# Performance work log

Measured on AMD Instinct MI355X. Metric: run time of the kernel, lower is better.

## Reference

```python
import jax, jax.numpy as jnp
import numpy as np

B, LA, LQ, LO, H, OUT = 32, 2048, 64, 32, 1024, 5


def _kaiming(key, out_f, in_f):
    return jax.random.normal(key, (out_f, in_f), jnp.float32) * np.sqrt(2.0 / in_f)


def setup_inputs() -> dict:
    key = jax.random.key(0)
    ks = jax.random.split(key, 16)
    inp = {
        "article_contexts": jax.random.normal(ks[0], (B, LA, H), jnp.float32),
        "question_contexts": jax.random.normal(ks[1], (B, LQ, H), jnp.float32),
        "options_embeds": jax.random.normal(ks[2], (B, 5, LO, H), jnp.float32),
        "answer_indices": jax.random.randint(ks[3], (B,), 0, LQ),
    }
    # mlp_att (article-question attention) params
    inp["a_Qw"], inp["a_Qb"] = _kaiming(ks[4], H, H), jnp.zeros((H,), jnp.float32)
    inp["a_Kw"], inp["a_Kb"] = _kaiming(ks[5], H, H), jnp.zeros((H,), jnp.float32)
    inp["a_Vw"], inp["a_Vb"] = _kaiming(ks[6], H, H), jnp.zeros((H,), jnp.float32)
    inp["a_vw"], inp["a_vb"] = _kaiming(ks[7], 1, H), jnp.zeros((1,), jnp.float32)
    # dot_layer (option attention) params
    inp["d_Qw"], inp["d_Qb"] = _kaiming(ks[8], H, H), jnp.zeros((H,), jnp.float32)
    inp["d_Kw"], inp["d_Kb"] = _kaiming(ks[9], H, H), jnp.zeros((H,), jnp.float32)
    inp["d_Vw"], inp["d_Vb"] = _kaiming(ks[10], H, H), jnp.zeros((H,), jnp.float32)
    inp["d_vw"], inp["d_vb"] = _kaiming(ks[11], 1, H), jnp.zeros((1,), jnp.float32)
    # final linear: hidden_size*5 -> output_dim
    inp["f_w"], inp["f_b"] = _kaiming(ks[12], OUT, 5 * H), jnp.zeros((OUT,), jnp.float32)
    return inp


def _mlp_att(Q, K, V, Qw, Qb, Kw, Kb, Vw, Vb, vw, vb):
    # Q: [B, H]; K, V: [B, (..opt..), L, H]. Dropout is identity (eval mode).
    Qp = Q @ Qw.T + Qb                      # [B, H]
    Kp = K @ Kw.T + Kb                      # [..., L, H]
    Vp = V @ Vw.T + Vb                      # [..., L, H]
    while Qp.ndim < Kp.ndim:
        Qp = Qp[..., None, :]
    M = jnp.tanh(Qp + Kp)                   # [..., L, H]
    scores = jax.nn.softmax(M @ vw.T + vb, axis=-2)  # softmax over L, [..., L, 1]
    return jnp.sum(Vp * scores, axis=-2)    # [..., H]


def reference(article_contexts, question_contexts, options_embeds, answer_indices,
              a_Qw, a_Qb, a_Kw, a_Kb, a_Vw, a_Vb, a_vw, a_vb,
              d_Qw, d_Qb, d_Kw, d_Kb, d_Vw, d_Vb, d_vw, d_vb,
              f_w, f_b):
    b = article_contexts.shape[0]
    # gather question context at the answer index -> [B, H]
    oqc = question_contexts[jnp.arange(b), answer_indices]
    # article-question additive attention -> [B, H]
    aq = _mlp_att(oqc, article_contexts, article_contexts,
                  a_Qw, a_Qb, a_Kw, a_Kb, a_Vw, a_Vb, a_vw, a_vb)
    # per-option additive attention, vectorized over the 5 options -> [B, 5, H]
    feats = _mlp_att(aq, options_embeds, options_embeds,
                     d_Qw, d_Qb, d_Kw, d_Kb, d_Vw, d_Vb, d_vw, d_vb)
    # concat options along feature dim, final linear -> [B, OUT]
    logits = feats.reshape(b, -1) @ f_w.T + f_b
    return logits
```

## Files before the change

### kernel.cpp

```cpp
#include <hip/hip_runtime.h>
#include <hip/hip_bf16.h>
#include <math.h>

#define HDIM 1024
#define NB 32
#define LA 2048
#define LO 32

typedef __attribute__((ext_vector_type(8))) short bf16x8;
typedef __attribute__((ext_vector_type(4))) float f32x4;
typedef unsigned int u32;

__device__ __forceinline__ float tanh_fast(float x){
    return 2.0f / (1.0f + __expf(-2.0f * x)) - 1.0f;
}

__device__ __forceinline__ void load_lds16(const void* gptr, void* lptr){
    __builtin_amdgcn_global_load_lds(
        (const __attribute__((address_space(1))) u32*)gptr,
        (__attribute__((address_space(3))) u32*)lptr, 16, 0, 0);
}

__global__ void zero_kernel(float* __restrict__ p, int n){
    int i = blockIdx.x * blockDim.x + threadIdx.x;
    int stride = gridDim.x * blockDim.x;
    for (; i < n; i += stride) p[i] = 0.0f;
}

__global__ void conv_bf16_kernel(const float* __restrict__ in, __hip_bfloat16* __restrict__ out, long n){
    long i = ((long)blockIdx.x * blockDim.x + threadIdx.x) * 4;
    long stride = (long)gridDim.x * blockDim.x * 4;
    for (; i < n; i += stride){
        float4 v = *(const float4*)(in + i);
        union { __hip_bfloat16 h[4]; short4 s; } u;
        u.h[0] = __float2bfloat16(v.x); u.h[1] = __float2bfloat16(v.y);
        u.h[2] = __float2bfloat16(v.z); u.h[3] = __float2bfloat16(v.w);
        *(short4*)(out + i) = u.s;
    }
}

__global__ void gather_kernel(const float* __restrict__ qc, const int* __restrict__ ans,
                              float* __restrict__ oqc){
    int b = blockIdx.x, tid = threadIdx.x;
    int idx = ans[b];
    const float* src = qc + ((size_t)b * 64 + idx) * HDIM;
    float* dst = oqc + (size_t)b * HDIM;
    #pragma unroll
    for (int l = 0; l < 4; l++) dst[tid + l * 256] = src[tid + l * 256];
}

__global__ __launch_bounds__(256) void proj_kernel(
    const float* __restrict__ in, const float* __restrict__ W,
    const float* __restrict__ bias, float* __restrict__ out){
    __shared__ float xin[HDIM];
    const int g = blockIdx.x, tid = threadIdx.x;
    const int lane = tid & 63, wave = tid >> 6;
    *(float4*)&xin[tid * 4] = *(const float4*)&in[(size_t)g * HDIM + tid * 4];
    __syncthreads();
    float4 xv[4];
    #pragma unroll
    for (int c = 0; c < 4; c++) xv[c] = *(const float4*)&xin[(c * 64 + lane) * 4];
    const int hbase = blockIdx.y * 64 + wave * 16;
    #pragma unroll 4
    for (int r = 0; r < 16; r++){
        int h = hbase + r;
        const float* Wr = W + (size_t)h * HDIM;
        float p = 0.f;
        #pragma unroll
        for (int c = 0; c < 4; c++){
            float4 wv = *(const float4*)&Wr[(c * 64 + lane) * 4];
            p = fmaf(xv[c].x, wv.x, p); p = fmaf(xv[c].y, wv.y, p);
            p = fmaf(xv[c].z, wv.z, p); p = fmaf(xv[c].w, wv.w, p);
        }
        #pragma unroll
        for (int off = 1; off < 64; off <<= 1) p += __shfl_xor(p, off, 64);
        if (lane == 0) out[(size_t)g * HDIM + h] = p + bias[h];
    }
}

#define NT 16
__global__ __launch_bounds__(512, 4) void score_mfma128_kernel(
    const __hip_bfloat16* __restrict__ X, const __hip_bfloat16* __restrict__ Kw,
    const float* __restrict__ Kb, const float* __restrict__ Qp,
    const float* __restrict__ vw, float* __restrict__ s,
    int row_off, int rows_per_batch)
{
    __shared__ __align__(16) char lds[65536];
    const int tid = threadIdx.x;
    const int lane = tid & 63, wid = tid >> 6;
    const int wm = wid >> 2, wn = wid & 3;
    const int lr = lane & 15, lg = lane >> 4;

    const int na = gridDim.x >> 3;
    const int per = na >> 3;
    const int bid = blockIdx.x;
    const int xcd = bid & 7, seq = bid >> 3;
    const int a_idx = xcd * per + (seq >> 3);
    const int h_idx = seq & 7;
    const int a0 = a_idx * 128;
    const int h0 = h_idx * 128;

    f32x4 acc[4][2] = {};

    const int rw_c0 = tid >> 3,  srcb_c0 = ((tid & 7) * 16) ^ ((rw_c0 & 7) << 4);
    const int rw_c1 = rw_c0 + 64, srcb_c1 = ((tid & 7) * 16) ^ ((rw_c1 & 7) << 4);
    const char* pA0 = (const char*)Kw + (size_t)(h0 + rw_c0) * 2048 + srcb_c0;
    const char* pA1 = (const char*)Kw + (size_t)(h0 + rw_c1) * 2048 + srcb_c1;
    const char* pB0 = (const char*)X  + (size_t)(a0 + rw_c0) * 2048 + srcb_c0;
    const char* pB1 = (const char*)X  + (size_t)(a0 + rw_c1) * 2048 + srcb_c1;
    char* dA0 = lds + tid * 16;
    char* dA1 = lds + 8192 + tid * 16;
    char* dB0 = lds + 32768 + tid * 16;
    char* dB1 = lds + 32768 + 8192 + tid * 16;

    int aoff[4][2], boff[2][2];
    #pragma unroll
    for (int hf = 0; hf < 4; hf++){
        int rw = wm * 64 + hf * 16 + lr;
        int o0 = rw * 128 + ((lg * 16) ^ ((rw & 7) << 4));
        aoff[hf][0] = o0; aoff[hf][1] = o0 ^ 64;
    }
    #pragma unroll
    for (int af = 0; af < 2; af++){
        int rw = wn * 32 + af * 16 + lr;
        int o0 = 32768 + rw * 128 + ((lg * 16) ^ ((rw & 7) << 4));
        boff[af][0] = o0; boff[af][1] = o0 ^ 64;
    }

#define STAGE_ADV(bufoff) do { \
    load_lds16(pA0, dA0 + (bufoff)); load_lds16(pA1, dA1 + (bufoff)); \
    load_lds16(pB0, dB0 + (bufoff)); load_lds16(pB1, dB1 + (bufoff)); \
    pA0 += 128; pA1 += 128; pB0 += 128; pB1 += 128; } while(0)

#define COMPUTE(bufoff) do { \
    _Pragma("unroll") \
    for (int ks = 0; ks < 2; ks++){ \
        bf16x8 av[4], bv[2]; \
        _Pragma("unroll") \
        for (int hf = 0; hf < 4; hf++) \
            av[hf] = *(const bf16x8*)(lds + (bufoff) + aoff[hf][ks]); \
        _Pragma("unroll") \
        for (int af = 0; af < 2; af++) \
            bv[af] = *(const bf16x8*)(lds + (bufoff) + boff[af][ks]); \
        __builtin_amdgcn_s_setprio(1); \
        _Pragma("unroll") \
        for (int hf = 0; hf < 4; hf++) \
            _Pragma("unroll") \
            for (int af = 0; af < 2; af++) \
                acc[hf][af] = __builtin_amdgcn_mfma_f32_16x16x32_bf16(av[hf], bv[af], acc[hf][af], 0, 0, 0); \
        __builtin_amdgcn_s_setprio(0); \
    } } while(0)

    STAGE_ADV(0);
    STAGE_ADV(16384);
    int bo = 0;
    for (int kt = 0; kt < NT - 1; ++kt){
        asm volatile("s_waitcnt vmcnt(4)" ::: "memory");
        __builtin_amdgcn_s_barrier();
        __builtin_amdgcn_sched_barrier(0);
        COMPUTE(bo);
        __builtin_amdgcn_s_barrier();
        if (kt < NT - 2) STAGE_ADV(bo);
        bo ^= 16384;
    }
    asm volatile("s_waitcnt vmcnt(0)" ::: "memory");
    __builtin_amdgcn_s_barrier();
    __builtin_amdgcn_sched_barrier(0);
    COMPUTE(bo);

    const int b = (row_off + a0) / rows_per_batch;
    float qv[4][4], vv[4][4];
    #pragma unroll
    for (int hf = 0; hf < 4; hf++){
        int hbase = h0 + wm * 64 + hf * 16 + lg * 4;
        float4 kb4 = *(const float4*)(Kb + hbase);
        float4 qp4 = *(const float4*)(Qp + (size_t)b * HDIM + hbase);
        float4 vw4 = *(const float4*)(vw + hbase);
        qv[hf][0] = kb4.x + qp4.x; qv[hf][1] = kb4.y + qp4.y;
        qv[hf][2] = kb4.z + qp4.z; qv[hf][3] = kb4.w + qp4.w;
        vv[hf][0] = vw4.x; vv[hf][1] = vw4.y; vv[hf][2] = vw4.z; vv[hf][3] = vw4.w;
    }
    #pragma unroll
    for (int af = 0; af < 2; af++){
        float sacc = 0.f;
        #pragma unroll
        for (int hf = 0; hf < 4; hf++)
            #pragma unroll
            for (int r = 0; r < 4; r++)
                sacc += tanh_fast(acc[hf][af][r] + qv[hf][r]) * vv[hf][r];
        sacc += __shfl_xor(sacc, 16, 64);
        sacc += __shfl_xor(sacc, 32, 64);
        if (lane < 16)
            atomicAdd(&s[row_off + a0 + wn * 32 + af * 16 + lr], sacc);
    }
#undef STAGE_ADV
#undef COMPUTE
}

#define SBM 128
#define SBN 128
__global__ __launch_bounds__(256) void score_mfma_kernel(
    const __hip_bfloat16* __restrict__ X, const __hip_bfloat16* __restrict__ Kw,
    const float* __restrict__ Kb, const float* __restrict__ Qp,
    const float* __restrict__ vw, float* __restrict__ s,
    int row_off, int rows_per_batch)
{
    __shared__ __align__(16) __hip_bfloat16 As[SBM][32];
    __shared__ __align__(16) __hip_bfloat16 Bs[SBN][32];
    const int tid = threadIdx.x;
    const int lane = tid & 63, wid = tid >> 6;
    const int wm = wid >> 1, wn = wid & 1;
    const int row0 = blockIdx.x * SBM;
    const int h0 = blockIdx.y * SBN;
    const int lr = lane & 15, lg = lane >> 4;

    f32x4 acc[4][4] = {};

    for (int k0 = 0; k0 < HDIM; k0 += 32){
        #pragma unroll
        for (int l = 0; l < 2; l++){
            int f = tid + l * 256;
            int r = f >> 2, c8 = (f & 3) * 8;
            load_lds16(X + (size_t)(row0 + r) * HDIM + k0 + c8, &As[0][0] + f * 8);
            load_lds16(Kw + (size_t)(h0 + r) * HDIM + k0 + c8, &Bs[0][0] + f * 8);
        }
        __syncthreads();
        bf16x8 a[4], b[4];
        #pragma unroll
        for (int i = 0; i < 4; i++)
            a[i] = *(const bf16x8*)&As[wm * 64 + i * 16 + lr][lg * 8];
        #pragma unroll
        for (int j = 0; j < 4; j++)
            b[j] = *(const bf16x8*)&Bs[wn * 64 + j * 16 + lr][lg * 8];
        #pragma unroll
        for (int i = 0; i < 4; i++)
            #pragma unroll
            for (int j = 0; j < 4; j++)
                acc[i][j] = __builtin_amdgcn_mfma_f32_16x16x32_bf16(a[i], b[j], acc[i][j], 0, 0, 0);
        __syncthreads();
    }

    float kbv[4], vwv[4];
    #pragma unroll
    for (int j = 0; j < 4; j++){
        int h = h0 + wn * 64 + j * 16 + lr;
        kbv[j] = Kb[h]; vwv[j] = vw[h];
    }
    #pragma unroll
    for (int i = 0; i < 4; i++){
        #pragma unroll
        for (int reg = 0; reg < 4; reg++){
            int r = row0 + wm * 64 + i * 16 + lg * 4 + reg;
            int gr = row_off + r;
            int bb = gr / rows_per_batch;
            const float* Qpb = Qp + (size_t)bb * HDIM;
            float p = 0.f;
            #pragma unroll
            for (int j = 0; j < 4; j++){
                int h = h0 + wn * 64 + j * 16 + lr;
                p += tanh_fast(acc[i][j][reg] + kbv[j] + Qpb[h]) * vwv[j];
            }
            #pragma unroll
            for (int off = 1; off < 16; off <<= 1) p += __shfl_xor(p, off, 16);
            if (lr == 0) atomicAdd(&s[gr], p);
        }
    }
}

__global__ void softmax_kernel(float* __restrict__ s, int Rg){
    __shared__ float red[4];
    int g = blockIdx.x, tid = threadIdx.x;
    float* sg = s + (size_t)g * Rg;
    float m = -INFINITY;
    for (int i = tid; i < Rg; i += 256) m = fmaxf(m, sg[i]);
    #pragma unroll
    for (int off = 32; off > 0; off >>= 1) m = fmaxf(m, __shfl_down(m, off, 64));
    if ((tid & 63) == 0) red[tid >> 6] = m;
    __syncthreads();
    m = fmaxf(fmaxf(red[0], red[1]), fmaxf(red[2], red[3]));
    __syncthreads();
    float sum = 0.f;
    for (int i = tid; i < Rg; i += 256){ float e = __expf(sg[i] - m); sg[i] = e; sum += e; }
    #pragma unroll
    for (int off = 32; off > 0; off >>= 1) sum += __shfl_down(sum, off, 64);
    if ((tid & 63) == 0) red[tid >> 6] = sum;
    __syncthreads();
    float inv = 1.0f / (red[0] + red[1] + red[2] + red[3]);
    for (int i = tid; i < Rg; i += 256) sg[i] *= inv;
}

__global__ void wsum_kernel(const float* __restrict__ X, const float* __restrict__ sc,
                            float* __restrict__ out, int Rg, int rowsPerChunk){
    __shared__ float scs[256];
    int g = blockIdx.x >> 2;
    int kc = blockIdx.x & 3;
    int i0 = blockIdx.y * rowsPerChunk;
    int tid = threadIdx.x;
    if (tid < rowsPerChunk) scs[tid] = sc[(size_t)g * Rg + i0 + tid];
    __syncthreads();
    int k = kc * 256 + tid;
    const float* Xg = X + ((size_t)g * Rg + i0) * HDIM + k;
    float acc = 0.f;
    for (int i = 0; i < rowsPerChunk; i++)
        acc += scs[i] * Xg[(size_t)i * HDIM];
    atomicAdd(&out[(size_t)g * HDIM + k], acc);
}

__global__ void wsum_bf16_kernel(const __hip_bfloat16* __restrict__ X, const float* __restrict__ sc,
                                 float* __restrict__ out, int Rg, int rowsPerChunk){
    __shared__ float scs[256];
    int g = blockIdx.x >> 2;
    int kc = blockIdx.x & 3;
    int i0 = blockIdx.y * rowsPerChunk;
    int tid = threadIdx.x;
    if (tid < rowsPerChunk) scs[tid] = sc[(size_t)g * Rg + i0 + tid];
    __syncthreads();
    int k = kc * 256 + tid;
    const __hip_bfloat16* Xg = X + ((size_t)g * Rg + i0) * HDIM + k;
    float acc = 0.f;
    for (int i = 0; i < rowsPerChunk; i++)
        acc += scs[i] * __bfloat162float(Xg[(size_t)i * HDIM]);
    atomicAdd(&out[(size_t)g * HDIM + k], acc);
}

__global__ void final_kernel(const float* __restrict__ feats, const float* __restrict__ fw,
                             const float* __restrict__ fb, float* __restrict__ out){
    __shared__ float red[4];
    int b = blockIdx.x, tid = threadIdx.x;
    const float* fe = feats + (size_t)b * 5120;
    for (int j = 0; j < 5; j++){
        float acc = 0.f;
        for (int i = tid; i < 5120; i += 256) acc += fe[i] * fw[(size_t)j * 5120 + i];
        #pragma unroll
        for (int off = 32; off > 0; off >>= 1) acc += __shfl_down(acc, off, 64);
        if ((tid & 63) == 0) red[tid >> 6] = acc;
        __syncthreads();
        if (tid == 0) out[b * 5 + j] = fb[j] + red[0] + red[1] + red[2] + red[3];
        __syncthreads();
    }
}

extern "C" void kernel_launch(void* const* d_in, const int* in_sizes, int n_in,
                              void* d_out, int out_size, void* d_ws, size_t ws_size,
                              hipStream_t stream) {
    const float* article  = (const float*)d_in[0];
    const float* question = (const float*)d_in[1];
    const float* options  = (const float*)d_in[2];
    const int*   ans      = (const int*)d_in[3];
    const float* a_Qw = (const float*)d_in[4];  const float* a_Qb = (const float*)d_in[5];
    const float* a_Kw = (const float*)d_in[6];  const float* a_Kb = (const float*)d_in[7];
    const float* a_Vw = (const float*)d_in[8];  const float* a_Vb = (const float*)d_in[9];
    const float* a_vw = (const float*)d_in[10];
    const float* d_Qw = (const float*)d_in[12]; const float* d_Qb = (const float*)d_in[13];
    const float* d_Kw = (const float*)d_in[14]; const float* d_Kb = (const float*)d_in[15];
    const float* d_Vw = (const float*)d_in[16]; const float* d_Vb = (const float*)d_in[17];
    const float* d_vw = (const float*)d_in[18];
    const float* f_w  = (const float*)d_in[20]; const float* f_b  = (const float*)d_in[21];
    float* out = (float*)d_out;

    float* ws = (float*)d_ws;
    float* oqc   = ws;
    float* qp_a  = ws + 32768;
    float* aq    = ws + 65536;
    float* qp_d  = ws + 98304;
    float* feats = ws + 131072;
    float* s_art = ws + 294912;
    float* s_opt = ws + 360448;
    float* w_art = ws + 365568;
    float* wd    = ws + 398336;
    __hip_bfloat16* kwa_bf = (__hip_bfloat16*)(ws + 562176);
    __hip_bfloat16* kwd_bf = kwa_bf + 1048576;
    __hip_bfloat16* opt_bf = kwd_bf + 1048576;
    __hip_bfloat16* art_bf = opt_bf + 5242880;
    size_t used_bytes = 562176 * 4 + (size_t)(1048576 * 2 + 5242880) * 2;
    long avail_rows = (long)((ws_size - used_bytes) / (HDIM * 2));
    int rows_total = NB * LA;
    int chunk_rows = (int)(avail_rows < rows_total ? avail_rows : rows_total);
    chunk_rows &= ~1023;
    if (chunk_rows < 1024) chunk_rows = 1024;

    zero_kernel<<<256, 256, 0, stream>>>(s_art, 267264);
    gather_kernel<<<NB, 256, 0, stream>>>(question, ans, oqc);
    proj_kernel<<<dim3(NB, 16), 256, 0, stream>>>(oqc, a_Qw, a_Qb, qp_a);
    conv_bf16_kernel<<<64, 256, 0, stream>>>(a_Kw, kwa_bf, 1048576);

    for (int r0 = 0; r0 < rows_total; r0 += chunk_rows){
        int nr = rows_total - r0; if (nr > chunk_rows) nr = chunk_rows;
        conv_bf16_kernel<<<1024, 256, 0, stream>>>(article + (size_t)r0 * HDIM, art_bf, (long)nr * HDIM);
        score_mfma128_kernel<<<(nr / 128) * 8, 512, 0, stream>>>(
            art_bf, kwa_bf, a_Kb, qp_a, a_vw, s_art, r0, LA);
    }
    softmax_kernel<<<NB, 256, 0, stream>>>(s_art, LA);
    if (chunk_rows >= rows_total)
        wsum_bf16_kernel<<<dim3(NB * 4, 8), 256, 0, stream>>>(art_bf, s_art, w_art, LA, 256);
    else
        wsum_kernel<<<dim3(NB * 4, 8), 256, 0, stream>>>(article, s_art, w_art, LA, 256);
    proj_kernel<<<dim3(NB, 16), 256, 0, stream>>>(w_art, a_Vw, a_Vb, aq);

    proj_kernel<<<dim3(NB, 16), 256, 0, stream>>>(aq, d_Qw, d_Qb, qp_d);
    conv_bf16_kernel<<<64, 256, 0, stream>>>(d_Kw, kwd_bf, 1048576);
    conv_bf16_kernel<<<320, 256, 0, stream>>>(options, opt_bf, 5242880);
    score_mfma_kernel<<<dim3((NB * 5 * LO) / SBM, HDIM / SBN), 256, 0, stream>>>(
        opt_bf, kwd_bf, d_Kb, qp_d, d_vw, s_opt, 0, 5 * LO);
    softmax_kernel<<<NB * 5, 256, 0, stream>>>(s_opt, LO);
    wsum_kernel<<<dim3(NB * 5 * 4, 1), 256, 0, stream>>>(options, s_opt, wd, LO, LO);
    proj_kernel<<<dim3(NB * 5, 16), 256, 0, stream>>>(wd, d_Vw, d_Vb, feats);
    final_kernel<<<NB, 256, 0, stream>>>(feats, f_w, f_b, out);
}
```

Baseline: 443.0 us.

## Enlarge article score GEMM tile to 128x256 with K=32 stages

The article scoring MFMA kernel now covers 256 article rows per block instead of 128, with each wave holding a 4x4 accumulator grid. The K step per stage drops from 64 to 32 (32 iterations), and the LDS swizzle is reworked for 64-byte rows, so double-buffered LDS use falls from 64KB to 48KB. The aim is more reuse of each loaded Kw tile and fewer blocks re-reading the weight matrix. The costs are more accumulator registers per thread and twice as many barrier-synchronised iterations; chunk rounding is raised to 2048 rows to match.

```diff
diff --git a/kernel.cpp b/kernel.cpp
--- a/kernel.cpp
+++ b/kernel.cpp
@@ -78,14 +78,14 @@
     }
 }
 
-#define NT 16
-__global__ __launch_bounds__(512, 4) void score_mfma128_kernel(
+#define NT 32
+__global__ __launch_bounds__(512, 4) void score_mfma_kA(
     const __hip_bfloat16* __restrict__ X, const __hip_bfloat16* __restrict__ Kw,
     const float* __restrict__ Kb, const float* __restrict__ Qp,
     const float* __restrict__ vw, float* __restrict__ s,
     int row_off, int rows_per_batch)
 {
-    __shared__ __align__(16) char lds[65536];
+    __shared__ __align__(16) char lds[49152];
     const int tid = threadIdx.x;
     const int lane = tid & 63, wid = tid >> 6;
     const int wm = wid >> 2, wn = wid & 3;
@@ -97,71 +97,66 @@
     const int xcd = bid & 7, seq = bid >> 3;
     const int a_idx = xcd * per + (seq >> 3);
     const int h_idx = seq & 7;
-    const int a0 = a_idx * 128;
+    const int a0 = a_idx * 256;
     const int h0 = h_idx * 128;
 
-    f32x4 acc[4][2] = {};
-
-    const int rw_c0 = tid >> 3,  srcb_c0 = ((tid & 7) * 16) ^ ((rw_c0 & 7) << 4);
-    const int rw_c1 = rw_c0 + 64, srcb_c1 = ((tid & 7) * 16) ^ ((rw_c1 & 7) << 4);
-    const char* pA0 = (const char*)Kw + (size_t)(h0 + rw_c0) * 2048 + srcb_c0;
-    const char* pA1 = (const char*)Kw + (size_t)(h0 + rw_c1) * 2048 + srcb_c1;
-    const char* pB0 = (const char*)X  + (size_t)(a0 + rw_c0) * 2048 + srcb_c0;
-    const char* pB1 = (const char*)X  + (size_t)(a0 + rw_c1) * 2048 + srcb_c1;
-    char* dA0 = lds + tid * 16;
-    char* dA1 = lds + 8192 + tid * 16;
-    char* dB0 = lds + 32768 + tid * 16;
-    char* dB1 = lds + 32768 + 8192 + tid * 16;
-
-    int aoff[4][2], boff[2][2];
+    f32x4 acc[4][4] = {};
+
+    const int rA  = tid >> 2;
+    const int kcA = ((tid & 3) ^ ((rA >> 1) & 3)) * 16;
+    const int rB1 = rA + 128;
+    const char* pA  = (const char*)Kw + (size_t)(h0 + rA) * 2048 + kcA;
+    const char* pB0 = (const char*)X  + (size_t)(a0 + rA) * 2048 + kcA;
+    const char* pB1 = (const char*)X  + (size_t)(a0 + rB1) * 2048 + kcA;
+    char* dA  = lds + tid * 16;
+    char* dB0 = lds + 8192 + tid * 16;
+    char* dB1 = lds + 16384 + tid * 16;
+
+    int aoff[4], boff[4];
     #pragma unroll
     for (int hf = 0; hf < 4; hf++){
         int rw = wm * 64 + hf * 16 + lr;
-        int o0 = rw * 128 + ((lg * 16) ^ ((rw & 7) << 4));
-        aoff[hf][0] = o0; aoff[hf][1] = o0 ^ 64;
-    }
-    #pragma unroll
-    for (int af = 0; af < 2; af++){
-        int rw = wn * 32 + af * 16 + lr;
-        int o0 = 32768 + rw * 128 + ((lg * 16) ^ ((rw & 7) << 4));
-        boff[af][0] = o0; boff[af][1] = o0 ^ 64;
+        aoff[hf] = rw * 64 + ((lg * 16) ^ (((rw >> 1) & 3) << 4));
+    }
+    #pragma unroll
+    for (int af = 0; af < 4; af++){
+        int rw = wn * 64 + af * 16 + lr;
+        boff[af] = 8192 + rw * 64 + ((lg * 16) ^ (((rw >> 1) & 3) << 4));
     }
 
 #define STAGE_ADV(bufoff) do { \
-    load_lds16(pA0, dA0 + (bufoff)); load_lds16(pA1, dA1 + (bufoff)); \
-    load_lds16(pB0, dB0 + (bufoff)); load_lds16(pB1, dB1 + (bufoff)); \
-    pA0 += 128; pA1 += 128; pB0 += 128; pB1 += 128; } while(0)
+    load_lds16(pA,  dA  + (bufoff)); \
+    load_lds16(pB0, dB0 + (bufoff)); \
+    load_lds16(pB1, dB1 + (bufoff)); \
+    pA += 64; pB0 += 64; pB1 += 64; } while(0)
 
 #define COMPUTE(bufoff) do { \
+    bf16x8 av[4], bv[4]; \
     _Pragma("unroll") \
-    for (int ks = 0; ks < 2; ks++){ \
-        bf16x8 av[4], bv[2]; \
+    for (int hf = 0; hf < 4; hf++) \
+        av[hf] = *(const bf16x8*)(lds + (bufoff) + aoff[hf]); \
+    _Pragma("unroll") \
+    for (int af = 0; af < 4; af++) \
+        bv[af] = *(const bf16x8*)(lds + (bufoff) + boff[af]); \
+    __builtin_amdgcn_s_setprio(1); \
+    _Pragma("unroll") \
+    for (int hf = 0; hf < 4; hf++) \
         _Pragma("unroll") \
-        for (int hf = 0; hf < 4; hf++) \
-            av[hf] = *(const bf16x8*)(lds + (bufoff) + aoff[hf][ks]); \
-        _Pragma("unroll") \
-        for (int af = 0; af < 2; af++) \
-            bv[af] = *(const bf16x8*)(lds + (bufoff) + boff[af][ks]); \
-        __builtin_amdgcn_s_setprio(1); \
-        _Pragma("unroll") \
-        for (int hf = 0; hf < 4; hf++) \
-            _Pragma("unroll") \
-            for (int af = 0; af < 2; af++) \
-                acc[hf][af] = __builtin_amdgcn_mfma_f32_16x16x32_bf16(av[hf], bv[af], acc[hf][af], 0, 0, 0); \
-        __builtin_amdgcn_s_setprio(0); \
-    } } while(0)
+        for (int af = 0; af < 4; af++) \
+            acc[hf][af] = __builtin_amdgcn_mfma_f32_16x16x32_bf16(av[hf], bv[af], acc[hf][af], 0, 0, 0); \
+    __builtin_amdgcn_s_setprio(0); } while(0)
 
     STAGE_ADV(0);
-    STAGE_ADV(16384);
+    STAGE_ADV(24576);
     int bo = 0;
     for (int kt = 0; kt < NT - 1; ++kt){
-        asm volatile("s_waitcnt vmcnt(4)" ::: "memory");
+        asm volatile("s_waitcnt vmcnt(3)" ::: "memory");
         __builtin_amdgcn_s_barrier();
         __builtin_amdgcn_sched_barrier(0);
         COMPUTE(bo);
         __builtin_amdgcn_s_barrier();
         if (kt < NT - 2) STAGE_ADV(bo);
-        bo ^= 16384;
+        bo ^= 24576;
     }
     asm volatile("s_waitcnt vmcnt(0)" ::: "memory");
     __builtin_amdgcn_s_barrier();
@@ -181,7 +176,7 @@
         vv[hf][0] = vw4.x; vv[hf][1] = vw4.y; vv[hf][2] = vw4.z; vv[hf][3] = vw4.w;
     }
     #pragma unroll
-    for (int af = 0; af < 2; af++){
+    for (int af = 0; af < 4; af++){
         float sacc = 0.f;
         #pragma unroll
         for (int hf = 0; hf < 4; hf++)
@@ -191,7 +186,7 @@
         sacc += __shfl_xor(sacc, 16, 64);
         sacc += __shfl_xor(sacc, 32, 64);
         if (lane < 16)
-            atomicAdd(&s[row_off + a0 + wn * 32 + af * 16 + lr], sacc);
+            atomicAdd(&s[row_off + a0 + wn * 64 + af * 16 + lr], sacc);
     }
 #undef STAGE_ADV
 #undef COMPUTE
@@ -376,8 +371,8 @@
     long avail_rows = (long)((ws_size - used_bytes) / (HDIM * 2));
     int rows_total = NB * LA;
     int chunk_rows = (int)(avail_rows < rows_total ? avail_rows : rows_total);
-    chunk_rows &= ~1023;
-    if (chunk_rows < 1024) chunk_rows = 1024;
+    chunk_rows &= ~2047;
+    if (chunk_rows < 2048) chunk_rows = 2048;
 
     zero_kernel<<<256, 256, 0, stream>>>(s_art, 267264);
     gather_kernel<<<NB, 256, 0, stream>>>(question, ans, oqc);
@@ -387,7 +382,7 @@
     for (int r0 = 0; r0 < rows_total; r0 += chunk_rows){
         int nr = rows_total - r0; if (nr > chunk_rows) nr = chunk_rows;
         conv_bf16_kernel<<<1024, 256, 0, stream>>>(article + (size_t)r0 * HDIM, art_bf, (long)nr * HDIM);
-        score_mfma128_kernel<<<(nr / 128) * 8, 512, 0, stream>>>(
+        score_mfma_kA<<<(nr / 256) * 8, 512, 0, stream>>>(
             art_bf, kwa_bf, a_Kb, qp_a, a_vw, s_art, r0, LA);
     }
     softmax_kernel<<<NB, 256, 0, stream>>>(s_art, LA);
```

New measurement: 446.2 us. Within noise of the previous version (+0.7%).
